# Kernel optimization log

Hardware: AMD Instinct MI355X
Metric: run time of the kernel (lower is better)

The kernel has to match this reference:

```python
import jax, jax.numpy as jnp
import numpy as np

DIM = 1024
NUM_HEADS = 16
HEAD_DIM = DIM // NUM_HEADS


def setup_inputs() -> dict:
    key = jax.random.key(0)
    k_x, k_q, k_k, k_v, k_o = jax.random.split(key, 5)
    B, L = 2, 2048
    scale = 1.0 / np.sqrt(DIM)
    x_bld = jax.random.normal(k_x, (B, L, DIM), dtype=jnp.float32)
    # LinearGeneral kernels: (in_features, num_heads, head_dim) for q/k/v,
    # (num_heads, head_dim, out_features) for out. Init ~ lecun_normal-ish scale.
    Wq = jax.random.normal(k_q, (DIM, NUM_HEADS, HEAD_DIM), dtype=jnp.float32) * scale
    Wk = jax.random.normal(k_k, (DIM, NUM_HEADS, HEAD_DIM), dtype=jnp.float32) * scale
    Wv = jax.random.normal(k_v, (DIM, NUM_HEADS, HEAD_DIM), dtype=jnp.float32) * scale
    Wo = jax.random.normal(k_o, (NUM_HEADS, HEAD_DIM, DIM), dtype=jnp.float32) * scale
    return {"x_bld": x_bld, "Wq": Wq, "Wk": Wk, "Wv": Wv, "Wo": Wo}


def reference(x_bld, Wq, Wk, Wv, Wo) -> jnp.ndarray:
    # Projections: [B,L,D] x [D,H,hd] -> [B,L,H,hd]
    q_blhd = jnp.einsum('bld,dhk->blhk', x_bld, Wq)
    k_blhd = jnp.einsum('bld,dhk->blhk', x_bld, Wk)
    v_blhd = jnp.einsum('bld,dhk->blhk', x_bld, Wv)
    # Scores: [B,H,L,L]
    attn_bhll = jnp.einsum('bqhd,bkhd->bhqk', q_blhd, k_blhd)
    attn_bhll = attn_bhll / jnp.sqrt(jnp.asarray(HEAD_DIM, dtype=attn_bhll.dtype))
    L = x_bld.shape[1]
    qi = jnp.arange(L)[:, None]
    ki = jnp.arange(L)[None, :]
    mask_ll = ki <= qi  # causal, no window
    neg_inf = jnp.finfo(attn_bhll.dtype).min
    attn_bhll = jnp.where(mask_ll[None, None, :, :], attn_bhll, neg_inf)
    attn_bhll = jax.nn.softmax(attn_bhll, axis=-1)
    y_blhd = jnp.einsum('bhqk,bkhd->bqhd', attn_bhll, v_blhd)
    # Output projection: contract (H, hd) -> D
    return jnp.einsum('blhk,hkd->bld', y_blhd, Wo)
```

## Files before the change

### kernel.cpp

```cpp
#include <hip/hip_runtime.h>
#include <hip/hip_bf16.h>

typedef __hip_bfloat16 bf16;
typedef __attribute__((ext_vector_type(8))) short short8;
typedef __attribute__((ext_vector_type(4))) float f32x4;

__device__ __forceinline__ float bfbits2f(unsigned short u) {
    return __uint_as_float(((unsigned int)u) << 16);
}
__device__ __forceinline__ unsigned short f2bfbits(float f) {
    union { float f; unsigned int u; } x;
    x.f = f;
    unsigned int r = x.u + 0x7FFFu + ((x.u >> 16) & 1u);
    return (unsigned short)(r >> 16);
}
__device__ __forceinline__ unsigned int pack_bf16x2(float lo, float hi) {
    unsigned int u0 = __float_as_uint(lo) + 0x8000u;
    unsigned int u1 = __float_as_uint(hi) + 0x8000u;
    return __builtin_amdgcn_perm(u1, u0, 0x07060302u);
}
__device__ __forceinline__ void async_copy16(const void* g, void* l) {
    __builtin_amdgcn_global_load_lds(
        (const __attribute__((address_space(1))) void*)g,
        (__attribute__((address_space(3))) void*)l, 16, 0, 0);
}
__device__ __forceinline__ bool sniff_bf16(const unsigned int* p, int lane) {
    unsigned int wd = p[lane];
    unsigned int e = (wd >> 7) & 0xFFu;
    return __popcll(__ballot(e >= 90u && e <= 150u)) > 40;
}

__global__ __launch_bounds__(256) void prep(
    const void* __restrict__ X, const void* __restrict__ W1,
    const void* __restrict__ W2, const void* __restrict__ W3,
    const void* __restrict__ W4, short* __restrict__ xb,
    short* __restrict__ O1, short* __restrict__ O2,
    short* __restrict__ O3, short* __restrict__ O4) {
    __shared__ float tbuf[32][33];
    const int bx = blockIdx.x;
    const int tid = threadIdx.x;
    const int lane = tid & 63;

    if (bx < 2048) {
        const bool isBf = sniff_bf16((const unsigned int*)X, lane);
        const int i = (bx * 256 + tid) * 8;
        if (isBf) {
            *(short8*)&xb[i] = *(const short8*)((const short*)X + i);
        } else {
            const float* xf = (const float*)X + i;
            float4 a = *(const float4*)xf;
            float4 b = *(const float4*)(xf + 4);
            short8 o;
            o[0] = (short)f2bfbits(a.x); o[1] = (short)f2bfbits(a.y);
            o[2] = (short)f2bfbits(a.z); o[3] = (short)f2bfbits(a.w);
            o[4] = (short)f2bfbits(b.x); o[5] = (short)f2bfbits(b.y);
            o[6] = (short)f2bfbits(b.z); o[7] = (short)f2bfbits(b.w);
            *(short8*)&xb[i] = o;
        }
    } else {
        const void* Ws[4] = {W1, W2, W3, W4};
        short* Os[4] = {O1, O2, O3, O4};
        const int t = bx - 2048;
        const int wsel = t >> 10;
        const int tile = t & 1023;
        const int bxt = tile & 31, byt = tile >> 5;
        const void* W = Ws[wsel];
        const bool isBf = sniff_bf16((const unsigned int*)W, lane);
        const float scale = (wsel == 0) ? 0.125f : 1.0f;
        short* O = Os[wsel];

        const int tx = tid & 31, ty = tid >> 5;
        const int gx = bxt * 32 + tx;
#pragma unroll
        for (int i = 0; i < 4; i++) {
            const int gy = byt * 32 + ty + i * 8;
            float v = isBf
                ? bfbits2f(((const unsigned short*)W)[(size_t)gy * 1024 + gx])
                : ((const float*)W)[(size_t)gy * 1024 + gx];
            tbuf[ty + i * 8][tx] = v * scale;
        }
        __syncthreads();
#pragma unroll
        for (int i = 0; i < 4; i++) {
            const int orow = bxt * 32 + ty + i * 8;
            const int ocol = byt * 32 + tx;
            O[(size_t)orow * 1024 + ocol] = (short)f2bfbits(tbuf[tx][ty + i * 8]);
        }
    }
}

__global__ __launch_bounds__(256) void transpose_v(const short* __restrict__ qkv,
                                                   short* __restrict__ VtG) {
    __shared__ short t[32][33];
    const int tx = threadIdx.x & 31, ty = threadIdx.x >> 5;
    const int b = blockIdx.z >> 4, h = blockIdx.z & 15;
    const int l0 = blockIdx.x * 32, d0 = blockIdx.y * 32;
#pragma unroll
    for (int i = 0; i < 4; i++) {
        const int l = l0 + ty + i * 8;
        t[ty + i * 8][tx] =
            qkv[(size_t)(b * 2048 + l) * 3072 + 2048 + h * 64 + d0 + tx];
    }
    __syncthreads();
    const int ptx = 2 * (tx & 15) + (tx >> 4);
#pragma unroll
    for (int i = 0; i < 4; i++) {
        const int d = d0 + ty + i * 8;
        VtG[((size_t)(b * 16 + h) * 64 + d) * 2048 + l0 + ptx] = t[tx][ty + i * 8];
    }
}

template <int BN>
__global__ __launch_bounds__(256) void gemm_async(const short* __restrict__ A,
                                                  const short* __restrict__ Bt,
                                                  void* __restrict__ C,
                                                  const unsigned int* __restrict__ xdet,
                                                  int M, int N, int K) {
    __shared__ short As[2][128 * 32];
    __shared__ short Bs[2][BN * 32];
    constexpr int NI = BN / 32;

    const int tid = threadIdx.x;
    const int lane = tid & 63;
    const int wv = __builtin_amdgcn_readfirstlane(tid >> 6);
    const int quad = lane >> 4, l16 = lane & 15;
    const int wr = wv >> 1, wc = wv & 1;
    const int m0 = blockIdx.y * 128, n0 = blockIdx.x * BN;

    const int gr = lane >> 2;
    const int gc = ((lane & 3) ^ ((lane >> 3) & 3)) * 8;

    const f32x4 zero = {0.f, 0.f, 0.f, 0.f};
    f32x4 acc[4][NI];
#pragma unroll
    for (int mi = 0; mi < 4; mi++)
#pragma unroll
        for (int ni = 0; ni < NI; ni++) acc[mi][ni] = zero;

    const short* aptr[2];
    const short* bptr[BN / 64];
#pragma unroll
    for (int t = 0; t < 2; t++)
        aptr[t] = A + (size_t)(m0 + t * 64 + wv * 16 + gr) * K + gc;
#pragma unroll
    for (int t = 0; t < BN / 64; t++)
        bptr[t] = Bt + (size_t)(n0 + t * 64 + wv * 16 + gr) * K + gc;

#pragma unroll
    for (int t = 0; t < 2; t++) async_copy16(aptr[t], &As[0][(t * 64 + wv * 16) * 32]);
#pragma unroll
    for (int t = 0; t < BN / 64; t++) async_copy16(bptr[t], &Bs[0][(t * 64 + wv * 16) * 32]);

    const int ss = (quad ^ ((l16 >> 1) & 3)) * 8;

    for (int k0 = 0; k0 < K; k0 += 32) {
        const int cur = (k0 >> 5) & 1;
        __syncthreads();
        if (k0 + 32 < K) {
            const int nxt = cur ^ 1;
#pragma unroll
            for (int t = 0; t < 2; t++)
                async_copy16(aptr[t] + k0 + 32, &As[nxt][(t * 64 + wv * 16) * 32]);
#pragma unroll
            for (int t = 0; t < BN / 64; t++)
                async_copy16(bptr[t] + k0 + 32, &Bs[nxt][(t * 64 + wv * 16) * 32]);
        }

        short8 af[4], bfv[NI];
#pragma unroll
        for (int mi = 0; mi < 4; mi++)
            af[mi] = *(const short8*)&As[cur][(wr * 64 + mi * 16 + l16) * 32 + ss];
#pragma unroll
        for (int ni = 0; ni < NI; ni++)
            bfv[ni] = *(const short8*)&Bs[cur][(wc * (BN / 2) + ni * 16 + l16) * 32 + ss];
#pragma unroll
        for (int mi = 0; mi < 4; mi++)
#pragma unroll
            for (int ni = 0; ni < NI; ni++)
                acc[mi][ni] = __builtin_amdgcn_mfma_f32_16x16x32_bf16(
                    af[mi], bfv[ni], acc[mi][ni], 0, 0, 0);
    }

    bool outBf = true;
    if (xdet) outBf = sniff_bf16(xdet, lane);
    if (outBf) {
        unsigned short* Cb = (unsigned short*)C;
#pragma unroll
        for (int mi = 0; mi < 4; mi++)
#pragma unroll
            for (int ni = 0; ni < NI; ni++)
#pragma unroll
                for (int r = 0; r < 4; r++) {
                    const int row = m0 + wr * 64 + mi * 16 + quad * 4 + r;
                    const int col = n0 + wc * (BN / 2) + ni * 16 + l16;
                    Cb[(size_t)row * N + col] = f2bfbits(acc[mi][ni][r]);
                }
    } else {
        float* Cf = (float*)C;
#pragma unroll
        for (int mi = 0; mi < 4; mi++)
#pragma unroll
            for (int ni = 0; ni < NI; ni++)
#pragma unroll
                for (int r = 0; r < 4; r++) {
                    const int row = m0 + wr * 64 + mi * 16 + quad * 4 + r;
                    const int col = n0 + wc * (BN / 2) + ni * 16 + l16;
                    Cf[(size_t)row * N + col] = acc[mi][ni][r];
                }
    }
}

__global__ __launch_bounds__(256) void attn_mfma6(
    const short* __restrict__ qkv, const short* __restrict__ VtG,
    short* __restrict__ Yg, short* __restrict__ Opart, float* __restrict__ ml) {
    __shared__ short Ks[2][64 * 64];
    __shared__ short Vt[2][64 * 64];
    __shared__ short Ps[2 * 64 * 32];

    const int tid = threadIdx.x;
    const int lane = tid & 63;
    const int wv = __builtin_amdgcn_readfirstlane(tid >> 6);
    const int quad = lane >> 4, l16 = lane & 15;
    const int bh = blockIdx.x;
    const int b = bh >> 4, h = bh & 15;

    int qb, seg, S;
    const int slot = blockIdx.y;
    if (slot < 64)      { qb = 31 - (slot >> 2); seg = slot & 3; S = 4; }
    else if (slot < 80) { const int t2 = slot - 64; qb = 15 - (t2 >> 1); seg = t2 & 1; S = 2; }
    else                { qb = 87 - slot; seg = 0; S = 1; }

    const int ns = qb + 1;
    const int sb0 = seg * ns / S;
    const int sb1 = (seg + 1) * ns / S;

    const int rr = lane >> 3;
    const int scol = ((lane & 7) ^ rr) * 8;

    const short* kptr[2];
    const short* vptr[2];
    short* kdst[2];
    short* vdst[2];
#pragma unroll
    for (int i = 0; i < 2; i++) {
        const int u = wv * 2 + i;
        kptr[i] = qkv + (size_t)(b * 2048 + sb0 * 64 + u * 8 + rr) * 3072 + 1024 +
                  h * 64 + scol;
        kdst[i] = &Ks[0][(u * 8) * 64];
        vptr[i] = VtG + ((size_t)bh * 64 + u * 8 + rr) * 2048 + sb0 * 64 + scol;
        vdst[i] = &Vt[0][(u * 8) * 64];
    }
    const int bufoff = 64 * 64;
    const int buf0 = sb0 & 1;
    const int qbuf = buf0 ^ 1;

#pragma unroll
    for (int i = 0; i < 2; i++) {
        const int u = wv * 2 + i;
        const short* qsrc = qkv + (size_t)(b * 2048 + qb * 64 + u * 8 + rr) * 3072 +
                            h * 64 + scol;
        async_copy16(qsrc, &Ks[qbuf][(u * 8) * 64]);
        async_copy16(kptr[i], kdst[i] + buf0 * bufoff);
        async_copy16(vptr[i], vdst[i] + buf0 * bufoff);
        kptr[i] += 64 * 3072;
        vptr[i] += 64;
    }
    __syncthreads();
    const int sl = (quad ^ (l16 & 7)) * 8;
    const short8 qf0 = *(const short8*)&Ks[qbuf][(wv * 16 + l16) * 64 + sl];
    const short8 qf1 = *(const short8*)&Ks[qbuf][(wv * 16 + l16) * 64 + (sl ^ 32)];
    __syncthreads();

    unsigned int* Psd = (unsigned int*)Ps;
    const f32x4 minit = {-12.f, -12.f, -12.f, -12.f};
    f32x4 O[4];
#pragma unroll
    for (int ni = 0; ni < 4; ni++) O[ni] = {0.f, 0.f, 0.f, 0.f};
    float l_st[4] = {0.f, 0.f, 0.f, 0.f};
    const int qrow0 = qb * 64 + wv * 16 + quad * 4;
    const int psl = (quad ^ ((l16 >> 2) & 3)) * 8;

    for (int sb = sb0; sb < sb1; sb++) {
        const int cur = sb & 1;
        if (sb != sb0) __syncthreads();
        if (sb + 1 < sb1) {
            const int nxt = cur ^ 1;
#pragma unroll
            for (int i = 0; i < 2; i++) {
                async_copy16(kptr[i], kdst[i] + nxt * bufoff);
                async_copy16(vptr[i], vdst[i] + nxt * bufoff);
                kptr[i] += 64 * 3072;
                vptr[i] += 64;
            }
        }
        const short* Kc = &Ks[cur][0];
        const short* Vc = &Vt[cur][0];

        f32x4 s[4];
#pragma unroll
        for (int ni = 0; ni < 4; ni++) {
            short8 kf0 = *(const short8*)&Kc[(ni * 16 + l16) * 64 + sl];
            short8 kf1 = *(const short8*)&Kc[(ni * 16 + l16) * 64 + (sl ^ 32)];
            s[ni] = __builtin_amdgcn_mfma_f32_16x16x32_bf16(qf0, kf0, minit, 0, 0, 0);
            s[ni] = __builtin_amdgcn_mfma_f32_16x16x32_bf16(qf1, kf1, s[ni], 0, 0, 0);
        }

        if (sb == qb) {
#pragma unroll
            for (int ni = 0; ni < 4; ni++) {
                const int key = sb * 64 + ni * 16 + l16;
#pragma unroll
                for (int r = 0; r < 4; r++)
                    if (key > qrow0 + r) s[ni][r] = -1e30f;
            }
        }

#pragma unroll
        for (int ni = 0; ni < 4; ni++)
#pragma unroll
            for (int r = 0; r < 4; r++) s[ni][r] = __expf(s[ni][r]);
#pragma unroll
        for (int r = 0; r < 4; r++)
            l_st[r] += (s[0][r] + s[1][r]) + (s[2][r] + s[3][r]);

#pragma unroll
        for (int c = 0; c < 2; c++)
#pragma unroll
            for (int r = 0; r < 4; r++)
                Psd[(c * 64 + wv * 16 + quad * 4 + r) * 16 + (l16 ^ (quad << 2))] =
                    pack_bf16x2(s[2 * c][r], s[2 * c + 1][r]);

        short8 pf[2];
#pragma unroll
        for (int c = 0; c < 2; c++)
            pf[c] = *(const short8*)&Ps[(c * 64 + wv * 16 + l16) * 32 + psl];

#pragma unroll
        for (int ni = 0; ni < 4; ni++)
#pragma unroll
            for (int c = 0; c < 2; c++) {
                short8 vf = *(const short8*)&Vc[(ni * 16 + l16) * 64 + (sl ^ (c << 5))];
                O[ni] = __builtin_amdgcn_mfma_f32_16x16x32_bf16(pf[c], vf, O[ni], 0, 0, 0);
            }
    }

    float lt[4];
#pragma unroll
    for (int r = 0; r < 4; r++) {
        float v = l_st[r];
        v += __shfl_xor(v, 1);
        v += __shfl_xor(v, 2);
        v += __shfl_xor(v, 4);
        v += __shfl_xor(v, 8);
        lt[r] = v;
    }

    if (S == 1) {
#pragma unroll
        for (int r = 0; r < 4; r++) {
            const float inv = 1.f / lt[r];
            const int qrow = qrow0 + r;
#pragma unroll
            for (int ni = 0; ni < 4; ni++)
                Yg[(size_t)(b * 2048 + qrow) * 1024 + h * 64 + ni * 16 + l16] =
                    (short)f2bfbits(O[ni][r] * inv);
        }
    } else {
        const int qidx = qb - 8;
        const int base = ((seg * 32 + bh) * 24 + qidx) * 64;
#pragma unroll
        for (int r = 0; r < 4; r++) {
            const int q = wv * 16 + quad * 4 + r;
#pragma unroll
            for (int ni = 0; ni < 4; ni++)
                Opart[(size_t)(base + q) * 64 + ni * 16 + l16] =
                    (short)f2bfbits(O[ni][r]);
            if (l16 == 0) ml[base + q] = lt[r];
        }
    }
}

__global__ __launch_bounds__(256) void attn_combine6(
    const short* __restrict__ Opart, const float* __restrict__ ml,
    short* __restrict__ Yg) {
    const int qb = 8 + blockIdx.x;
    const int bh = blockIdx.y;
    const int b = bh >> 4, h = bh & 15;
    const int S = (qb >= 16) ? 4 : 2;
    const int qidx = qb - 8;
    const int tid = threadIdx.x;
    const int q = tid >> 2;
    const int d0 = (tid & 3) * 16;

    float a0[8] = {}, a1[8] = {};
    float lsum = 0.f;
    for (int s = 0; s < S; s++) {
        const int idx = ((s * 32 + bh) * 24 + qidx) * 64 + q;
        lsum += ml[idx];
        const short* p = Opart + (size_t)idx * 64 + d0;
        short8 x0 = *(const short8*)p;
        short8 x1 = *(const short8*)(p + 8);
#pragma unroll
        for (int t = 0; t < 8; t++) {
            a0[t] += bfbits2f((unsigned short)x0[t]);
            a1[t] += bfbits2f((unsigned short)x1[t]);
        }
    }
    const float inv = 1.f / lsum;
    short8 o0, o1;
#pragma unroll
    for (int t = 0; t < 8; t++) {
        o0[t] = (short)f2bfbits(a0[t] * inv);
        o1[t] = (short)f2bfbits(a1[t] * inv);
    }
    short* yp = Yg + (size_t)(b * 2048 + qb * 64 + q) * 1024 + h * 64 + d0;
    *(short8*)yp = o0;
    *(short8*)(yp + 8) = o1;
}

extern "C" void kernel_launch(void* const* d_in, const int* in_sizes, int n_in,
                              void* d_out, int out_size, void* d_ws, size_t ws_size,
                              hipStream_t stream) {
    const int M = 2 * 2048;
    const int D = 1024;

    char* w = (char*)d_ws;
    short* xb  = (short*)w;
    short* WqT = (short*)(w + (8u << 20));
    short* WkT = WqT + (1u << 20);
    short* WvT = WkT + (1u << 20);
    short* WoT = WvT + (1u << 20);
    short* qkv = WoT + (1u << 20);
    short* VtG = qkv + (size_t)M * 3072;
    short* Opart = VtG + (size_t)2048 * 2048;
    float* mlp = (float*)(Opart + (size_t)4 * 32 * 24 * 64 * 64);
    short* y = xb;

    prep<<<6144, 256, 0, stream>>>(d_in[0], d_in[1], d_in[2], d_in[3], d_in[4],
                                   xb, WqT, WkT, WvT, WoT);

    gemm_async<128><<<dim3(3072 / 128, M / 128), 256, 0, stream>>>(
        xb, WqT, qkv, nullptr, M, 3072, D);

    transpose_v<<<dim3(64, 2, 32), 256, 0, stream>>>(qkv, VtG);

    attn_mfma6<<<dim3(32, 88), 256, 0, stream>>>(qkv, VtG, y, Opart, mlp);
    attn_combine6<<<dim3(24, 32), 256, 0, stream>>>(Opart, mlp, y);

    gemm_async<64><<<dim3(D / 64, M / 128), 256, 0, stream>>>(
        y, WoT, d_out, (const unsigned int*)d_in[0], M, D, D);
}
```

Baseline: 184.5 us.

## Restructure attention to register-resident K/V with transposed score MFMA and 2-wave key split

```diff
diff --git a/kernel.cpp b/kernel.cpp
--- a/kernel.cpp
+++ b/kernel.cpp
@@ -4,6 +4,7 @@
 typedef __hip_bfloat16 bf16;
 typedef __attribute__((ext_vector_type(8))) short short8;
 typedef __attribute__((ext_vector_type(4))) float f32x4;
+typedef __attribute__((ext_vector_type(4))) unsigned int u32x4;
 
 __device__ __forceinline__ float bfbits2f(unsigned short u) {
     return __uint_as_float(((unsigned int)u) << 16);
@@ -66,7 +67,7 @@
         const int bxt = tile & 31, byt = tile >> 5;
         const void* W = Ws[wsel];
         const bool isBf = sniff_bf16((const unsigned int*)W, lane);
-        const float scale = (wsel == 0) ? 0.125f : 1.0f;
+        const float scale = (wsel == 0) ? 0.18033688f : 1.0f;
         short* O = Os[wsel];
 
         const int tx = tid & 31, ty = tid >> 5;
@@ -210,12 +211,11 @@
     }
 }
 
-__global__ __launch_bounds__(256) void attn_mfma6(
+__global__ __launch_bounds__(128) void attn_mfma8(
     const short* __restrict__ qkv, const short* __restrict__ VtG,
     short* __restrict__ Yg, short* __restrict__ Opart, float* __restrict__ ml) {
-    __shared__ short Ks[2][64 * 64];
-    __shared__ short Vt[2][64 * 64];
-    __shared__ short Ps[2 * 64 * 32];
+    __shared__ float scr[4][16][68];
+    __shared__ float lred[2][64];
 
     const int tid = threadIdx.x;
     const int lane = tid & 63;
@@ -233,149 +233,159 @@
     const int ns = qb + 1;
     const int sb0 = seg * ns / S;
     const int sb1 = (seg + 1) * ns / S;
-
-    const int rr = lane >> 3;
-    const int scol = ((lane & 7) ^ rr) * 8;
-
-    const short* kptr[2];
-    const short* vptr[2];
-    short* kdst[2];
-    short* vdst[2];
-#pragma unroll
-    for (int i = 0; i < 2; i++) {
-        const int u = wv * 2 + i;
-        kptr[i] = qkv + (size_t)(b * 2048 + sb0 * 64 + u * 8 + rr) * 3072 + 1024 +
-                  h * 64 + scol;
-        kdst[i] = &Ks[0][(u * 8) * 64];
-        vptr[i] = VtG + ((size_t)bh * 64 + u * 8 + rr) * 2048 + sb0 * 64 + scol;
-        vdst[i] = &Vt[0][(u * 8) * 64];
-    }
-    const int bufoff = 64 * 64;
-    const int buf0 = sb0 & 1;
-    const int qbuf = buf0 ^ 1;
-
-#pragma unroll
-    for (int i = 0; i < 2; i++) {
-        const int u = wv * 2 + i;
-        const short* qsrc = qkv + (size_t)(b * 2048 + qb * 64 + u * 8 + rr) * 3072 +
-                            h * 64 + scol;
-        async_copy16(qsrc, &Ks[qbuf][(u * 8) * 64]);
-        async_copy16(kptr[i], kdst[i] + buf0 * bufoff);
-        async_copy16(vptr[i], vdst[i] + buf0 * bufoff);
-        kptr[i] += 64 * 3072;
-        vptr[i] += 64;
+    const int w32 = wv * 32;
+
+    short8 qf[4][2];
+    {
+        const short* qbase = qkv + (size_t)(b * 2048 + qb * 64 + l16) * 3072 +
+                             h * 64 + quad * 8;
+#pragma unroll
+        for (int qt = 0; qt < 4; qt++)
+#pragma unroll
+            for (int hf = 0; hf < 2; hf++)
+                qf[qt][hf] = *(const short8*)(qbase + qt * 16 * 3072 + hf * 32);
+    }
+
+    const size_t KSTEP = (size_t)64 * 3072;
+    const short* kb[2];
+#pragma unroll
+    for (int kt = 0; kt < 2; kt++)
+        kb[kt] = qkv + (size_t)(b * 2048 + sb0 * 64 + w32 + kt * 16 + l16) * 3072 +
+                 1024 + h * 64 + quad * 8;
+    const short* vb[4];
+#pragma unroll
+    for (int dt = 0; dt < 4; dt++)
+        vb[dt] = VtG + ((size_t)bh * 64 + dt * 16 + l16) * 2048 + sb0 * 64 + w32 +
+                 quad * 8;
+
+    f32x4 O[4][4];
+#pragma unroll
+    for (int qt = 0; qt < 4; qt++)
+#pragma unroll
+        for (int dt = 0; dt < 4; dt++) O[qt][dt] = {0.f, 0.f, 0.f, 0.f};
+    float lp[4] = {0.f, 0.f, 0.f, 0.f};
+
+    const f32x4 minit = {-17.3123405f, -17.3123405f, -17.3123405f, -17.3123405f};
+    const int keyoff0 = w32 + quad * 4;
+
+    auto LOADK = [&](short8 (&kf)[2][2], short8 (&vf)[4]) {
+#pragma unroll
+        for (int kt = 0; kt < 2; kt++) {
+#pragma unroll
+            for (int hf = 0; hf < 2; hf++)
+                kf[kt][hf] = *(const short8*)(kb[kt] + hf * 32);
+            kb[kt] += KSTEP;
+        }
+#pragma unroll
+        for (int dt = 0; dt < 4; dt++) {
+            vf[dt] = *(const short8*)vb[dt];
+            vb[dt] += 64;
+        }
+    };
+
+    auto COMPUTE = [&](const short8 (&kf)[2][2], const short8 (&vf)[4], int sb) {
+#pragma unroll
+        for (int qt = 0; qt < 4; qt++) {
+            f32x4 sA = __builtin_amdgcn_mfma_f32_16x16x32_bf16(kf[0][0], qf[qt][0], minit, 0, 0, 0);
+            sA = __builtin_amdgcn_mfma_f32_16x16x32_bf16(kf[0][1], qf[qt][1], sA, 0, 0, 0);
+            f32x4 sB = __builtin_amdgcn_mfma_f32_16x16x32_bf16(kf[1][0], qf[qt][0], minit, 0, 0, 0);
+            sB = __builtin_amdgcn_mfma_f32_16x16x32_bf16(kf[1][1], qf[qt][1], sB, 0, 0, 0);
+            if (sb == qb) {
+                const int qcol = qt * 16 + l16;
+#pragma unroll
+                for (int r = 0; r < 4; r++) {
+                    if (keyoff0 + r > qcol) sA[r] = -1e30f;
+                    if (keyoff0 + 16 + r > qcol) sB[r] = -1e30f;
+                }
+            }
+            union { u32x4 u; short8 s; } pa;
+#pragma unroll
+            for (int t = 0; t < 4; t++) {
+                sA[t] = __builtin_amdgcn_exp2f(sA[t]);
+                sB[t] = __builtin_amdgcn_exp2f(sB[t]);
+                lp[qt] += sA[t] + sB[t];
+                pa.u[t] = pack_bf16x2(sA[t], sB[t]);
+            }
+#pragma unroll
+            for (int dt = 0; dt < 4; dt++)
+                O[qt][dt] = __builtin_amdgcn_mfma_f32_16x16x32_bf16(
+                    pa.s, vf[dt], O[qt][dt], 0, 0, 0);
+        }
+    };
+
+    short8 kA[2][2], vA[4], kB[2][2], vB[4];
+    LOADK(kA, vA);
+    int sb = sb0;
+    while (true) {
+        if (sb + 1 < sb1) LOADK(kB, vB);
+        COMPUTE(kA, vA, sb);
+        if (++sb >= sb1) break;
+        if (sb + 1 < sb1) LOADK(kA, vA);
+        COMPUTE(kB, vB, sb);
+        if (++sb >= sb1) break;
+    }
+
+#pragma unroll
+    for (int qt = 0; qt < 4; qt++) {
+        float v = lp[qt];
+        v += __shfl_xor(v, 16);
+        v += __shfl_xor(v, 32);
+        if (quad == 0) lred[wv][qt * 16 + l16] = v;
+    }
+
+#pragma unroll
+    for (int qt = 0; qt < 4; qt++) {
+        if ((qt >> 1) != wv) {
+#pragma unroll
+            for (int dt = 0; dt < 4; dt++)
+#pragma unroll
+                for (int r = 0; r < 4; r++)
+                    scr[qt][quad * 4 + r][dt * 16 + l16] = O[qt][dt][r];
+        }
     }
     __syncthreads();
-    const int sl = (quad ^ (l16 & 7)) * 8;
-    const short8 qf0 = *(const short8*)&Ks[qbuf][(wv * 16 + l16) * 64 + sl];
-    const short8 qf1 = *(const short8*)&Ks[qbuf][(wv * 16 + l16) * 64 + (sl ^ 32)];
-    __syncthreads();
-
-    unsigned int* Psd = (unsigned int*)Ps;
-    const f32x4 minit = {-12.f, -12.f, -12.f, -12.f};
-    f32x4 O[4];
-#pragma unroll
-    for (int ni = 0; ni < 4; ni++) O[ni] = {0.f, 0.f, 0.f, 0.f};
-    float l_st[4] = {0.f, 0.f, 0.f, 0.f};
-    const int qrow0 = qb * 64 + wv * 16 + quad * 4;
-    const int psl = (quad ^ ((l16 >> 2) & 3)) * 8;
-
-    for (int sb = sb0; sb < sb1; sb++) {
-        const int cur = sb & 1;
-        if (sb != sb0) __syncthreads();
-        if (sb + 1 < sb1) {
-            const int nxt = cur ^ 1;
-#pragma unroll
-            for (int i = 0; i < 2; i++) {
-                async_copy16(kptr[i], kdst[i] + nxt * bufoff);
-                async_copy16(vptr[i], vdst[i] + nxt * bufoff);
-                kptr[i] += 64 * 3072;
-                vptr[i] += 64;
+#pragma unroll
+    for (int qt = 0; qt < 4; qt++) {
+        if ((qt >> 1) == wv) {
+#pragma unroll
+            for (int dt = 0; dt < 4; dt++)
+#pragma unroll
+                for (int r = 0; r < 4; r++)
+                    O[qt][dt][r] += scr[qt][quad * 4 + r][dt * 16 + l16];
+        }
+    }
+
+    if (S == 1) {
+#pragma unroll
+        for (int qt = 0; qt < 4; qt++) {
+            if ((qt >> 1) == wv) {
+#pragma unroll
+                for (int r = 0; r < 4; r++) {
+                    const int q = qt * 16 + quad * 4 + r;
+                    const float inv = 1.f / (lred[0][q] + lred[1][q]);
+#pragma unroll
+                    for (int dt = 0; dt < 4; dt++)
+                        Yg[(size_t)(b * 2048 + qb * 64 + q) * 1024 + h * 64 +
+                           dt * 16 + l16] = (short)f2bfbits(O[qt][dt][r] * inv);
+                }
             }
-        }
-        const short* Kc = &Ks[cur][0];
-        const short* Vc = &Vt[cur][0];
-
-        f32x4 s[4];
-#pragma unroll
-        for (int ni = 0; ni < 4; ni++) {
-            short8 kf0 = *(const short8*)&Kc[(ni * 16 + l16) * 64 + sl];
-            short8 kf1 = *(const short8*)&Kc[(ni * 16 + l16) * 64 + (sl ^ 32)];
-            s[ni] = __builtin_amdgcn_mfma_f32_16x16x32_bf16(qf0, kf0, minit, 0, 0, 0);
-            s[ni] = __builtin_amdgcn_mfma_f32_16x16x32_bf16(qf1, kf1, s[ni], 0, 0, 0);
-        }
-
-        if (sb == qb) {
-#pragma unroll
-            for (int ni = 0; ni < 4; ni++) {
-                const int key = sb * 64 + ni * 16 + l16;
-#pragma unroll
-                for (int r = 0; r < 4; r++)
-                    if (key > qrow0 + r) s[ni][r] = -1e30f;
-            }
-        }
-
-#pragma unroll
-        for (int ni = 0; ni < 4; ni++)
-#pragma unroll
-            for (int r = 0; r < 4; r++) s[ni][r] = __expf(s[ni][r]);
-#pragma unroll
-        for (int r = 0; r < 4; r++)
-            l_st[r] += (s[0][r] + s[1][r]) + (s[2][r] + s[3][r]);
-
-#pragma unroll
-        for (int c = 0; c < 2; c++)
-#pragma unroll
-            for (int r = 0; r < 4; r++)
-                Psd[(c * 64 + wv * 16 + quad * 4 + r) * 16 + (l16 ^ (quad << 2))] =
-                    pack_bf16x2(s[2 * c][r], s[2 * c + 1][r]);
-
-        short8 pf[2];
-#pragma unroll
-        for (int c = 0; c < 2; c++)
-            pf[c] = *(const short8*)&Ps[(c * 64 + wv * 16 + l16) * 32 + psl];
-
-#pragma unroll
-        for (int ni = 0; ni < 4; ni++)
-#pragma unroll
-            for (int c = 0; c < 2; c++) {
-                short8 vf = *(const short8*)&Vc[(ni * 16 + l16) * 64 + (sl ^ (c << 5))];
-                O[ni] = __builtin_amdgcn_mfma_f32_16x16x32_bf16(pf[c], vf, O[ni], 0, 0, 0);
-            }
-    }
-
-    float lt[4];
-#pragma unroll
-    for (int r = 0; r < 4; r++) {
-        float v = l_st[r];
-        v += __shfl_xor(v, 1);
-        v += __shfl_xor(v, 2);
-        v += __shfl_xor(v, 4);
-        v += __shfl_xor(v, 8);
-        lt[r] = v;
-    }
-
-    if (S == 1) {
-#pragma unroll
-        for (int r = 0; r < 4; r++) {
-            const float inv = 1.f / lt[r];
-            const int qrow = qrow0 + r;
-#pragma unroll
-            for (int ni = 0; ni < 4; ni++)
-                Yg[(size_t)(b * 2048 + qrow) * 1024 + h * 64 + ni * 16 + l16] =
-                    (short)f2bfbits(O[ni][r] * inv);
         }
     } else {
         const int qidx = qb - 8;
         const int base = ((seg * 32 + bh) * 24 + qidx) * 64;
 #pragma unroll
-        for (int r = 0; r < 4; r++) {
-            const int q = wv * 16 + quad * 4 + r;
-#pragma unroll
-            for (int ni = 0; ni < 4; ni++)
-                Opart[(size_t)(base + q) * 64 + ni * 16 + l16] =
-                    (short)f2bfbits(O[ni][r]);
-            if (l16 == 0) ml[base + q] = lt[r];
+        for (int qt = 0; qt < 4; qt++) {
+            if ((qt >> 1) == wv) {
+#pragma unroll
+                for (int r = 0; r < 4; r++) {
+                    const int q = qt * 16 + quad * 4 + r;
+#pragma unroll
+                    for (int dt = 0; dt < 4; dt++)
+                        Opart[(size_t)(base + q) * 64 + dt * 16 + l16] =
+                            (short)f2bfbits(O[qt][dt][r]);
+                    if (l16 == 0) ml[base + q] = lred[0][q] + lred[1][q];
+                }
+            }
         }
     }
 }
@@ -444,7 +454,7 @@
 
     transpose_v<<<dim3(64, 2, 32), 256, 0, stream>>>(qkv, VtG);
 
-    attn_mfma6<<<dim3(32, 88), 256, 0, stream>>>(qkv, VtG, y, Opart, mlp);
+    attn_mfma8<<<dim3(32, 88), 128, 0, stream>>>(qkv, VtG, y, Opart, mlp);
     attn_combine6<<<dim3(24, 32), 256, 0, stream>>>(Opart, mlp, y);
 
     gemm_async<64><<<dim3(D / 64, M / 128), 256, 0, stream>>>(
```

Result: slower. 209.7 us (+13.7%).
